# Kernel tuning notes

Hardware: AMD Instinct MI355X
Metric: run time of the kernel (lower is better)

Reference implementation:

```python
import jax, jax.numpy as jnp
import numpy as np

D = 4096
NB = 4
DFF = int(D * (4 / 3))  # 5461
EPS = 1e-5


def _ln(x, g, b):
    mu = jnp.mean(x, axis=-1, keepdims=True)
    var = jnp.var(x, axis=-1, keepdims=True)
    return (x - mu) * jax.lax.rsqrt(var + EPS) * g + b


def setup_inputs() -> dict:
    key = jax.random.key(0)
    ks = jax.random.split(key, 8)
    bs = NB  # blocks
    ib = D // NB
    inp = {
        "x": jax.random.normal(ks[0], (4, 2048, D), jnp.float32),
        "W_gates": jax.random.normal(ks[1], (4, bs, ib, ib), jnp.float32) / np.sqrt(ib),
        "b_gates": jnp.zeros((4, D), jnp.float32),
        "Wr_gates": jax.random.normal(ks[2], (4, bs, ib, ib), jnp.float32) / np.sqrt(ib),
        "ln_gamma": jnp.ones((8, D), jnp.float32),
        "ln_beta": jnp.zeros((8, D), jnp.float32),
        "lnout_gamma": jnp.ones((DFF,), jnp.float32),
        "lnout_beta": jnp.zeros((DFF,), jnp.float32),
        "W_left": jax.random.normal(ks[3], (DFF, D), jnp.float32) / np.sqrt(D),
        "b_left": jnp.zeros((DFF,), jnp.float32),
        "W_right": jax.random.normal(ks[4], (DFF, D), jnp.float32) / np.sqrt(D),
        "b_right": jnp.zeros((DFF,), jnp.float32),
        "W_proj": jax.random.normal(ks[5], (D, DFF), jnp.float32) / np.sqrt(DFF),
        "b_proj": jnp.zeros((D,), jnp.float32),
    }
    return inp


def reference(x, W_gates, b_gates, Wr_gates, ln_gamma, ln_beta,
              lnout_gamma, lnout_beta, W_left, b_left, W_right, b_right,
              W_proj, b_proj):
    B, N, Dm = x.shape
    nb = W_gates.shape[1]
    ib = Dm // nb

    # fresh states (init_states): all zeros
    ht_1 = jnp.zeros((B, N, Dm), x.dtype)

    xa = jax.nn.silu(x)
    xr = xa.reshape(B, N, nb, ib)
    hr = ht_1.reshape(B, N, nb, ib)
    # block-diagonal gate projections for all 4 gates (i, f, o, z) at once
    pre = jnp.einsum('bnki,gkoi->gbnko', xr, W_gates).reshape(4, B, N, Dm)
    pre = pre + jnp.einsum('bnki,gkoi->gbnko', hr, Wr_gates).reshape(4, B, N, Dm)
    pre = pre + b_gates[:, None, None, :]

    log_i = _ln(pre[0], ln_gamma[0], ln_beta[0])  # log of i before stabilization
    log_f = _ln(pre[1], ln_gamma[1], ln_beta[1])
    # stabilizer (mt_1 = 0): m = max(log f + mt_1, log i)
    m = jnp.maximum(log_f, log_i)
    i = jnp.exp(log_i - m)
    f = jnp.exp(log_f - m)

    o = jax.nn.sigmoid(_ln(pre[2], ln_gamma[2], ln_beta[2]))
    z = jnp.tanh(_ln(pre[3], ln_gamma[3], ln_beta[3]))

    # ct_1 = 0, nt_1 = 0
    ct = i * z
    ct = jnp.mean(_ln(ct, ln_gamma[4], ln_beta[4]), axis=(0, 1), keepdims=True)  # [1,1,D]
    nt = i
    nt = jnp.mean(_ln(nt, ln_gamma[5], ln_beta[5]), axis=(0, 1), keepdims=True)  # [1,1,D]

    ht = o * (ct / nt)  # broadcast [B,N,D]
    ht = jnp.mean(_ln(ht, ln_gamma[6], ln_beta[6]), axis=(0, 1), keepdims=True)  # [1,1,D]

    slstm_out = _ln(ht, ln_gamma[7], ln_beta[7])  # GN
    left = slstm_out @ W_left.T + b_left
    right = jax.nn.gelu(slstm_out @ W_right.T + b_right, approximate=False)
    out = _ln(left * right, lnout_gamma, lnout_beta)
    out = out @ W_proj.T + b_proj  # [1,1,hidden]
    return out
```

## Files before the change

kernel.cpp:

```cpp
#include <hip/hip_runtime.h>
#include <hip/hip_bf16.h>
#include <math.h>

#define DMODEL 4096
#define NROWS  8192
#define DFF    5461
#define CHUNK  512
#define NCHUNK 16
#define LNEPS  1e-5f

#define GBM 128
#define GBN 128
#define GBK 32
#define LOSCALE 2048.0f
#define LOINV   4.8828125e-4f

typedef _Float16 h8 __attribute__((ext_vector_type(8)));
typedef _Float16 h4 __attribute__((ext_vector_type(4)));
typedef float floatx4 __attribute__((ext_vector_type(4)));

__device__ inline unsigned short f2bf(float f) {
    unsigned int x = __builtin_bit_cast(unsigned int, f);
    unsigned int r = x + 0x7FFFu + ((x >> 16) & 1u);
    return (unsigned short)(r >> 16);
}
__device__ inline float bf2f(unsigned short u) {
    return __builtin_bit_cast(float, ((unsigned int)u) << 16);
}

#define GLL(gp, lp) __builtin_amdgcn_global_load_lds( \
    (const __attribute__((address_space(1))) void*)(gp), \
    (__attribute__((address_space(3))) void*)(lp), 16, 0, 0)

__global__ __launch_bounds__(256) void silu_split_k(const float* __restrict__ x,
                                                    _Float16* __restrict__ xh,
                                                    _Float16* __restrict__ xl) {
    size_t i = (size_t)blockIdx.x * 256 + threadIdx.x;
    float4 v = ((const float4*)x)[i];
    float s[4];
    s[0] = v.x / (1.f + expf(-v.x));
    s[1] = v.y / (1.f + expf(-v.y));
    s[2] = v.z / (1.f + expf(-v.z));
    s[3] = v.w / (1.f + expf(-v.w));
    h4 hi, lo;
#pragma unroll
    for (int j = 0; j < 4; ++j) {
        _Float16 h = (_Float16)s[j];
        hi[j] = h;
        lo[j] = (_Float16)((s[j] - (float)h) * LOSCALE);
    }
    ((h4*)xh)[i] = hi;
    ((h4*)xl)[i] = lo;
}

__global__ __launch_bounds__(256) void wsplit_k(const float* __restrict__ Wg,
                                                _Float16* __restrict__ wh,
                                                _Float16* __restrict__ wl) {
    size_t i = (size_t)blockIdx.x * 256 + threadIdx.x;
    float4 v = ((const float4*)Wg)[i];
    float s[4] = {v.x, v.y, v.z, v.w};
    h4 hi, lo;
#pragma unroll
    for (int j = 0; j < 4; ++j) {
        _Float16 h = (_Float16)s[j];
        hi[j] = h;
        lo[j] = (_Float16)((s[j] - (float)h) * LOSCALE);
    }
    ((h4*)wh)[i] = hi;
    ((h4*)wl)[i] = lo;
}

__global__ __launch_bounds__(256, 2) void gemm_split_k(
    const _Float16* __restrict__ xh, const _Float16* __restrict__ xl,
    const _Float16* __restrict__ wh, const _Float16* __restrict__ wl,
    float* __restrict__ pre, int row0)
{
    __shared__ __align__(16) _Float16 Ah[GBM * GBK];
    __shared__ __align__(16) _Float16 Al[GBM * GBK];
    __shared__ __align__(16) _Float16 Bh[GBN * GBK];
    __shared__ __align__(16) _Float16 Bl[GBN * GBK];

    const int gz = blockIdx.z;
    const int kb = gz & 3, g = gz >> 2;
    const int tM = blockIdx.y, tN = blockIdx.x;
    const int t = threadIdx.x;
    const int w = t >> 6, l = t & 63;
    const int lane15 = l & 15, quad = l >> 4;
    const int wm = w >> 1, wn = w & 1;

    const size_t Aoff = (size_t)(row0 + tM * GBM) * DMODEL + kb * 1024;
    const size_t Boff = (size_t)gz * (1024 * 1024) + (size_t)(tN * GBN) * 1024;

    floatx4 acc_h[4][4] = {};
    floatx4 acc_x[4][4] = {};

    for (int kt = 0; kt < 1024; kt += GBK) {
        const _Float16* ahs = xh + Aoff + kt;
        const _Float16* als = xl + Aoff + kt;
        const _Float16* bhs = wh + Boff + kt;
        const _Float16* bls = wl + Boff + kt;
#pragma unroll
        for (int it = 0; it < 2; ++it) {
            const int chunk = it * 256 + t;
            const int r = chunk >> 2;
            const int c = (chunk & 3) * 8;
            const int lo = (it * 256 + w * 64) * 8;
            const size_t ga = (size_t)r * DMODEL + c;
            const size_t gb = (size_t)r * 1024 + c;
            GLL(ahs + ga, Ah + lo);
            GLL(als + ga, Al + lo);
            GLL(bhs + gb, Bh + lo);
            GLL(bls + gb, Bl + lo);
        }
        __syncthreads();

        h8 af[4], alf[4], bf[4], blf[4];
#pragma unroll
        for (int mi = 0; mi < 4; ++mi) {
            const int ro = (wm * 64 + mi * 16 + lane15) * GBK + quad * 8;
            af[mi]  = *(const h8*)&Ah[ro];
            alf[mi] = *(const h8*)&Al[ro];
        }
#pragma unroll
        for (int ni = 0; ni < 4; ++ni) {
            const int ro = (wn * 64 + ni * 16 + lane15) * GBK + quad * 8;
            bf[ni]  = *(const h8*)&Bh[ro];
            blf[ni] = *(const h8*)&Bl[ro];
        }
#pragma unroll
        for (int mi = 0; mi < 4; ++mi)
#pragma unroll
            for (int ni = 0; ni < 4; ++ni) {
                acc_h[mi][ni] = __builtin_amdgcn_mfma_f32_16x16x32_f16(
                    af[mi], bf[ni], acc_h[mi][ni], 0, 0, 0);
                acc_x[mi][ni] = __builtin_amdgcn_mfma_f32_16x16x32_f16(
                    af[mi], blf[ni], acc_x[mi][ni], 0, 0, 0);
                acc_x[mi][ni] = __builtin_amdgcn_mfma_f32_16x16x32_f16(
                    alf[mi], bf[ni], acc_x[mi][ni], 0, 0, 0);
            }
        __syncthreads();
    }

#pragma unroll
    for (int mi = 0; mi < 4; ++mi) {
#pragma unroll
        for (int r = 0; r < 4; ++r) {
            const int rowl = tM * GBM + wm * 64 + mi * 16 + quad * 4 + r;
            float* dst = pre + ((size_t)g * CHUNK + rowl) * DMODEL
                         + kb * 1024 + tN * GBN + wn * 64 + lane15;
#pragma unroll
            for (int ni = 0; ni < 4; ++ni)
                dst[ni * 16] = acc_h[mi][ni][r] + acc_x[mi][ni][r] * LOINV;
        }
    }
}

template <int N>
__device__ inline void block_reduce(float* s, float* red) {
    const int t = threadIdx.x, w = t >> 6, l = t & 63;
#pragma unroll
    for (int i = 0; i < N; ++i) {
        float v = s[i];
#pragma unroll
        for (int off = 32; off > 0; off >>= 1) v += __shfl_xor(v, off, 64);
        if (l == 0) red[w * N + i] = v;
    }
    __syncthreads();
#pragma unroll
    for (int i = 0; i < N; ++i)
        s[i] = red[0 * N + i] + red[1 * N + i] + red[2 * N + i] + red[3 * N + i];
    __syncthreads();
}

#define EROWS 2
__global__ __launch_bounds__(256) void lnpass_k(
    const float* __restrict__ pre, const float* __restrict__ bg,
    const float* __restrict__ lng, const float* __restrict__ lnb,
    unsigned short* __restrict__ obuf,
    float* __restrict__ ctv, float* __restrict__ ntv, int row0)
{
    __shared__ float red[32];
    const int t = threadIdx.x;
    const float n1 = 1.f / DMODEL;
    float ct_acc[16] = {}, nt_acc[16] = {};

    for (int rr = 0; rr < EROWS; ++rr) {
        const int rl = blockIdx.x * EROWS + rr;
        const float* p0 = pre + ((size_t)0 * CHUNK + rl) * DMODEL;
        const float* p1 = pre + ((size_t)1 * CHUNK + rl) * DMODEL;
        const float* p2 = pre + ((size_t)2 * CHUNK + rl) * DMODEL;
        const float* p3 = pre + ((size_t)3 * CHUNK + rl) * DMODEL;

        float s[8] = {};
        for (int j = 0; j < 16; ++j) {
            const int d = t + 256 * j;
            float v0 = p0[d] + bg[d];
            float v1 = p1[d] + bg[DMODEL + d];
            float v2 = p2[d] + bg[2 * DMODEL + d];
            float v3 = p3[d] + bg[3 * DMODEL + d];
            s[0] += v0; s[1] += v0 * v0;
            s[2] += v1; s[3] += v1 * v1;
            s[4] += v2; s[5] += v2 * v2;
            s[6] += v3; s[7] += v3 * v3;
        }
        block_reduce<8>(s, red);
        const float mu0 = s[0] * n1, rs0 = rsqrtf(s[1] * n1 - mu0 * mu0 + LNEPS);
        const float mu1 = s[2] * n1, rs1 = rsqrtf(s[3] * n1 - mu1 * mu1 + LNEPS);
        const float mu2 = s[4] * n1, rs2 = rsqrtf(s[5] * n1 - mu2 * mu2 + LNEPS);
        const float mu3 = s[6] * n1, rs3 = rsqrtf(s[7] * n1 - mu3 * mu3 + LNEPS);

        float ctl[16], ntl[16];
        float s2[4] = {};
        for (int j = 0; j < 16; ++j) {
            const int d = t + 256 * j;
            float li = (p0[d] + bg[d] - mu0) * rs0 * lng[d] + lnb[d];
            float lf = (p1[d] + bg[DMODEL + d] - mu1) * rs1 * lng[DMODEL + d] + lnb[DMODEL + d];
            float iv = expf(fminf(li - lf, 0.f));
            float zv = tanhf((p3[d] + bg[3 * DMODEL + d] - mu3) * rs3 * lng[3 * DMODEL + d]
                             + lnb[3 * DMODEL + d]);
            float c = iv * zv;
            ctl[j] = c; ntl[j] = iv;
            s2[0] += c;  s2[1] += c * c;
            s2[2] += iv; s2[3] += iv * iv;
        }
        block_reduce<4>(s2, red);
        const float cmu = s2[0] * n1, crs = rsqrtf(s2[1] * n1 - cmu * cmu + LNEPS);
        const float nmu = s2[2] * n1, nrs = rsqrtf(s2[3] * n1 - nmu * nmu + LNEPS);

        for (int j = 0; j < 16; ++j) {
            const int d = t + 256 * j;
            ct_acc[j] += (ctl[j] - cmu) * crs * lng[4 * DMODEL + d] + lnb[4 * DMODEL + d];
            nt_acc[j] += (ntl[j] - nmu) * nrs * lng[5 * DMODEL + d] + lnb[5 * DMODEL + d];
            float ov = (p2[d] + bg[2 * DMODEL + d] - mu2) * rs2 * lng[2 * DMODEL + d]
                       + lnb[2 * DMODEL + d];
            ov = 1.f / (1.f + expf(-ov));
            obuf[(size_t)(row0 + rl) * DMODEL + d] = f2bf(ov);
        }
    }
    for (int j = 0; j < 16; ++j) {
        const int d = t + 256 * j;
        atomicAdd(&ctv[d], ct_acc[j]);
        atomicAdd(&ntv[d], nt_acc[j]);
    }
}

#define HROWS 16
__global__ __launch_bounds__(256) void htpass_k(
    const unsigned short* __restrict__ obuf,
    const float* __restrict__ ctv, const float* __restrict__ ntv,
    const float* __restrict__ lng, const float* __restrict__ lnb,
    float* __restrict__ htv)
{
    __shared__ float red[8];
    const int t = threadIdx.x;
    const float n1 = 1.f / DMODEL;
    float r[16], hacc[16] = {};
    for (int j = 0; j < 16; ++j) {
        const int d = t + 256 * j;
        r[j] = ctv[d] / ntv[d];
    }
    for (int rr = 0; rr < HROWS; ++rr) {
        const int row = blockIdx.x * HROWS + rr;
        float h[16]; float s[2] = {};
        for (int j = 0; j < 16; ++j) {
            const int d = t + 256 * j;
            h[j] = bf2f(obuf[(size_t)row * DMODEL + d]) * r[j];
            s[0] += h[j]; s[1] += h[j] * h[j];
        }
        block_reduce<2>(s, red);
        const float mu = s[0] * n1, rsv = rsqrtf(s[1] * n1 - mu * mu + LNEPS);
        for (int j = 0; j < 16; ++j) {
            const int d = t + 256 * j;
            hacc[j] += (h[j] - mu) * rsv * lng[6 * DMODEL + d] + lnb[6 * DMODEL + d];
        }
    }
    for (int j = 0; j < 16; ++j) {
        const int d = t + 256 * j;
        atomicAdd(&htv[d], hacc[j]);
    }
}

__global__ __launch_bounds__(256) void finalvec_k(
    const float* __restrict__ htv, const float* __restrict__ lng,
    const float* __restrict__ lnb, float* __restrict__ sout)
{
    __shared__ float red[8];
    const int t = threadIdx.x;
    const float n1 = 1.f / DMODEL;
    float v[16]; float s[2] = {};
    for (int j = 0; j < 16; ++j) {
        const int d = t + 256 * j;
        v[j] = htv[d] * (1.f / (float)NROWS);
        s[0] += v[j]; s[1] += v[j] * v[j];
    }
    block_reduce<2>(s, red);
    const float mu = s[0] * n1, rs = rsqrtf(s[1] * n1 - mu * mu + LNEPS);
    for (int j = 0; j < 16; ++j) {
        const int d = t + 256 * j;
        sout[d] = (v[j] - mu) * rs * lng[7 * DMODEL + d] + lnb[7 * DMODEL + d];
    }
}

__global__ __launch_bounds__(256) void ffn1_k(
    const float* __restrict__ sout,
    const float* __restrict__ Wl, const float* __restrict__ bl,
    const float* __restrict__ Wr, const float* __restrict__ br,
    float* __restrict__ u)
{
    const int t = threadIdx.x, w = t >> 6, l = t & 63;
    const int f = blockIdx.x * 4 + w;
    if (f >= DFF) return;
    const float4* wl4 = (const float4*)(Wl + (size_t)f * DMODEL);
    const float4* wr4 = (const float4*)(Wr + (size_t)f * DMODEL);
    const float4* s4 = (const float4*)sout;
    float a = 0.f, b = 0.f;
#pragma unroll
    for (int jj = 0; jj < 16; ++jj) {
        const int i4 = l + 64 * jj;
        float4 sv = s4[i4], av = wl4[i4], bv = wr4[i4];
        a += sv.x * av.x + sv.y * av.y + sv.z * av.z + sv.w * av.w;
        b += sv.x * bv.x + sv.y * bv.y + sv.z * bv.z + sv.w * bv.w;
    }
#pragma unroll
    for (int off = 32; off > 0; off >>= 1) {
        a += __shfl_xor(a, off, 64);
        b += __shfl_xor(b, off, 64);
    }
    if (l == 0) {
        float lv = a + bl[f];
        float rv = b + br[f];
        float g = 0.5f * rv * (1.f + erff(rv * 0.70710678118654752f));
        u[f] = lv * g;
    }
}

__global__ __launch_bounds__(256) void lnout_k(
    const float* __restrict__ u, const float* __restrict__ g,
    const float* __restrict__ b, float* __restrict__ y)
{
    __shared__ float red[8];
    const int t = threadIdx.x;
    float s[2] = {};
    for (int d = t; d < DFF; d += 256) { float v = u[d]; s[0] += v; s[1] += v * v; }
    block_reduce<2>(s, red);
    const float n1 = 1.f / (float)DFF;
    const float mu = s[0] * n1, rs = rsqrtf(s[1] * n1 - mu * mu + LNEPS);
    for (int d = t; d < DFF; d += 256) y[d] = (u[d] - mu) * rs * g[d] + b[d];
}

__global__ __launch_bounds__(256) void ffn2_k(
    const float* __restrict__ y, const float* __restrict__ Wp,
    const float* __restrict__ bp, float* __restrict__ out)
{
    const int t = threadIdx.x, w = t >> 6, l = t & 63;
    const int d = blockIdx.x * 4 + w;
    const float* row = Wp + (size_t)d * DFF;
    float s = 0.f;
    for (int j = l; j < DFF; j += 64) s += row[j] * y[j];
#pragma unroll
    for (int off = 32; off > 0; off >>= 1) s += __shfl_xor(s, off, 64);
    if (l == 0) out[d] = s + bp[d];
}

extern "C" void kernel_launch(void* const* d_in, const int* in_sizes, int n_in,
                              void* d_out, int out_size, void* d_ws, size_t ws_size,
                              hipStream_t stream)
{
    const float* x   = (const float*)d_in[0];
    const float* Wg  = (const float*)d_in[1];
    const float* bg  = (const float*)d_in[2];
    const float* lng = (const float*)d_in[4];
    const float* lnb = (const float*)d_in[5];
    const float* log_ = (const float*)d_in[6];
    const float* lob  = (const float*)d_in[7];
    const float* Wl  = (const float*)d_in[8];
    const float* bl  = (const float*)d_in[9];
    const float* Wr  = (const float*)d_in[10];
    const float* br  = (const float*)d_in[11];
    const float* Wp  = (const float*)d_in[12];
    const float* bp  = (const float*)d_in[13];
    float* out = (float*)d_out;

    char* ws = (char*)d_ws;
    size_t off = 0;
    _Float16* xh = (_Float16*)(ws + off); off += (size_t)NROWS * DMODEL * 2;
    _Float16* xl = (_Float16*)(ws + off); off += (size_t)NROWS * DMODEL * 2;
    _Float16* whp = (_Float16*)(ws + off); off += (size_t)16 * 1024 * 1024 * 2;
    _Float16* wlp = (_Float16*)(ws + off); off += (size_t)16 * 1024 * 1024 * 2;
    float* pre  = (float*)(ws + off); off += (size_t)4 * CHUNK * DMODEL * 4;
    float* ctv  = (float*)(ws + off); off += DMODEL * 4;
    float* ntv  = (float*)(ws + off); off += DMODEL * 4;
    float* htv  = (float*)(ws + off); off += DMODEL * 4;
    float* sout = (float*)(ws + off); off += DMODEL * 4;
    float* u    = (float*)(ws + off); off += DFF * 4;
    float* y    = (float*)(ws + off); off += DFF * 4;

    unsigned short* obuf = (unsigned short*)xl;

    hipMemsetAsync(ctv, 0, 3 * DMODEL * 4, stream);

    silu_split_k<<<(NROWS * DMODEL) / 1024, 256, 0, stream>>>(x, xh, xl);
    wsplit_k<<<(16 * 1024 * 1024) / 1024, 256, 0, stream>>>(Wg, whp, wlp);

    for (int c = 0; c < NCHUNK; ++c) {
        const int row0 = c * CHUNK;
        dim3 grid(1024 / GBN, CHUNK / GBM, 16);
        gemm_split_k<<<grid, 256, 0, stream>>>(xh, xl, whp, wlp, pre, row0);
        lnpass_k<<<CHUNK / EROWS, 256, 0, stream>>>(pre, bg, lng, lnb, obuf, ctv, ntv, row0);
    }

    htpass_k<<<NROWS / HROWS, 256, 0, stream>>>(obuf, ctv, ntv, lng, lnb, htv);
    finalvec_k<<<1, 256, 0, stream>>>(htv, lng, lnb, sout);
    ffn1_k<<<(DFF + 3) / 4, 256, 0, stream>>>(sout, Wl, bl, Wr, br, u);
    lnout_k<<<1, 256, 0, stream>>>(u, log_, lob, y);
    ffn2_k<<<DMODEL / 4, 256, 0, stream>>>(y, Wp, bp, out);

    (void)in_sizes; (void)n_in; (void)out_size; (void)ws_size;
}
```

Before: 2.636 ms.

## Use 1024-thread row blocks with float4 loads and shadow atomic accumulators

The LN pass and the ht pass now use 1024-thread blocks that handle one row, or four rows for the ht pass, with float4/ushort4 vectorized loads and stores instead of strided scalar accesses. The column accumulators for ct, nt and ht are replicated into four shadow copies indexed by block, so concurrent atomics spread across more addresses; consumers sum the copies. The aim is to cut memory transaction count and atomic contention. In exchange, lnpass issues more atomics in total (one row per block instead of two), and block reductions now span 16 waves.

```diff
diff --git a/kernel.cpp b/kernel.cpp
--- a/kernel.cpp
+++ b/kernel.cpp
@@ -8,6 +8,7 @@
 #define CHUNK  512
 #define NCHUNK 16
 #define LNEPS  1e-5f
+#define NSHADOW 4
 
 #define GBM 128
 #define GBN 128
@@ -156,6 +157,27 @@
 }
 
 template <int N>
+__device__ inline void block_reduce16(float* s, float* red) {
+    const int t = threadIdx.x, w = t >> 6, l = t & 63;
+#pragma unroll
+    for (int i = 0; i < N; ++i) {
+        float v = s[i];
+#pragma unroll
+        for (int off = 32; off > 0; off >>= 1) v += __shfl_xor(v, off, 64);
+        if (l == 0) red[w * N + i] = v;
+    }
+    __syncthreads();
+#pragma unroll
+    for (int i = 0; i < N; ++i) {
+        float acc = 0.f;
+#pragma unroll
+        for (int ww = 0; ww < 16; ++ww) acc += red[ww * N + i];
+        s[i] = acc;
+    }
+    __syncthreads();
+}
+
+template <int N>
 __device__ inline void block_reduce(float* s, float* red) {
     const int t = threadIdx.x, w = t >> 6, l = t & 63;
 #pragma unroll
@@ -172,112 +194,140 @@
     __syncthreads();
 }
 
-#define EROWS 2
-__global__ __launch_bounds__(256) void lnpass_k(
+__global__ __launch_bounds__(1024) void lnpass_k(
     const float* __restrict__ pre, const float* __restrict__ bg,
     const float* __restrict__ lng, const float* __restrict__ lnb,
     unsigned short* __restrict__ obuf,
     float* __restrict__ ctv, float* __restrict__ ntv, int row0)
 {
-    __shared__ float red[32];
+    __shared__ float red[16 * 8];
     const int t = threadIdx.x;
+    const int rl = blockIdx.x;
     const float n1 = 1.f / DMODEL;
-    float ct_acc[16] = {}, nt_acc[16] = {};
-
-    for (int rr = 0; rr < EROWS; ++rr) {
-        const int rl = blockIdx.x * EROWS + rr;
-        const float* p0 = pre + ((size_t)0 * CHUNK + rl) * DMODEL;
-        const float* p1 = pre + ((size_t)1 * CHUNK + rl) * DMODEL;
-        const float* p2 = pre + ((size_t)2 * CHUNK + rl) * DMODEL;
-        const float* p3 = pre + ((size_t)3 * CHUNK + rl) * DMODEL;
-
-        float s[8] = {};
-        for (int j = 0; j < 16; ++j) {
-            const int d = t + 256 * j;
-            float v0 = p0[d] + bg[d];
-            float v1 = p1[d] + bg[DMODEL + d];
-            float v2 = p2[d] + bg[2 * DMODEL + d];
-            float v3 = p3[d] + bg[3 * DMODEL + d];
-            s[0] += v0; s[1] += v0 * v0;
-            s[2] += v1; s[3] += v1 * v1;
-            s[4] += v2; s[5] += v2 * v2;
-            s[6] += v3; s[7] += v3 * v3;
-        }
-        block_reduce<8>(s, red);
-        const float mu0 = s[0] * n1, rs0 = rsqrtf(s[1] * n1 - mu0 * mu0 + LNEPS);
-        const float mu1 = s[2] * n1, rs1 = rsqrtf(s[3] * n1 - mu1 * mu1 + LNEPS);
-        const float mu2 = s[4] * n1, rs2 = rsqrtf(s[5] * n1 - mu2 * mu2 + LNEPS);
-        const float mu3 = s[6] * n1, rs3 = rsqrtf(s[7] * n1 - mu3 * mu3 + LNEPS);
-
-        float ctl[16], ntl[16];
-        float s2[4] = {};
-        for (int j = 0; j < 16; ++j) {
-            const int d = t + 256 * j;
-            float li = (p0[d] + bg[d] - mu0) * rs0 * lng[d] + lnb[d];
-            float lf = (p1[d] + bg[DMODEL + d] - mu1) * rs1 * lng[DMODEL + d] + lnb[DMODEL + d];
-            float iv = expf(fminf(li - lf, 0.f));
-            float zv = tanhf((p3[d] + bg[3 * DMODEL + d] - mu3) * rs3 * lng[3 * DMODEL + d]
-                             + lnb[3 * DMODEL + d]);
-            float c = iv * zv;
-            ctl[j] = c; ntl[j] = iv;
-            s2[0] += c;  s2[1] += c * c;
-            s2[2] += iv; s2[3] += iv * iv;
-        }
-        block_reduce<4>(s2, red);
-        const float cmu = s2[0] * n1, crs = rsqrtf(s2[1] * n1 - cmu * cmu + LNEPS);
-        const float nmu = s2[2] * n1, nrs = rsqrtf(s2[3] * n1 - nmu * nmu + LNEPS);
-
-        for (int j = 0; j < 16; ++j) {
-            const int d = t + 256 * j;
-            ct_acc[j] += (ctl[j] - cmu) * crs * lng[4 * DMODEL + d] + lnb[4 * DMODEL + d];
-            nt_acc[j] += (ntl[j] - nmu) * nrs * lng[5 * DMODEL + d] + lnb[5 * DMODEL + d];
-            float ov = (p2[d] + bg[2 * DMODEL + d] - mu2) * rs2 * lng[2 * DMODEL + d]
-                       + lnb[2 * DMODEL + d];
-            ov = 1.f / (1.f + expf(-ov));
-            obuf[(size_t)(row0 + rl) * DMODEL + d] = f2bf(ov);
-        }
-    }
-    for (int j = 0; j < 16; ++j) {
-        const int d = t + 256 * j;
-        atomicAdd(&ctv[d], ct_acc[j]);
-        atomicAdd(&ntv[d], nt_acc[j]);
-    }
-}
-
-#define HROWS 16
-__global__ __launch_bounds__(256) void htpass_k(
+
+    float v[4][4];
+#pragma unroll
+    for (int g = 0; g < 4; ++g) {
+        float4 pv = ((const float4*)(pre + ((size_t)g * CHUNK + rl) * DMODEL))[t];
+        float4 bv = ((const float4*)bg)[g * (DMODEL / 4) + t];
+        v[g][0] = pv.x + bv.x; v[g][1] = pv.y + bv.y;
+        v[g][2] = pv.z + bv.z; v[g][3] = pv.w + bv.w;
+    }
+
+    float s[8];
+#pragma unroll
+    for (int g = 0; g < 4; ++g) {
+        s[2 * g]     = v[g][0] + v[g][1] + v[g][2] + v[g][3];
+        s[2 * g + 1] = v[g][0] * v[g][0] + v[g][1] * v[g][1]
+                     + v[g][2] * v[g][2] + v[g][3] * v[g][3];
+    }
+    block_reduce16<8>(s, red);
+    const float mu0 = s[0] * n1, rs0 = rsqrtf(s[1] * n1 - mu0 * mu0 + LNEPS);
+    const float mu1 = s[2] * n1, rs1 = rsqrtf(s[3] * n1 - mu1 * mu1 + LNEPS);
+    const float mu2 = s[4] * n1, rs2 = rsqrtf(s[5] * n1 - mu2 * mu2 + LNEPS);
+    const float mu3 = s[6] * n1, rs3 = rsqrtf(s[7] * n1 - mu3 * mu3 + LNEPS);
+
+    float4 g0 = ((const float4*)lng)[0 * (DMODEL / 4) + t], b0 = ((const float4*)lnb)[0 * (DMODEL / 4) + t];
+    float4 g1 = ((const float4*)lng)[1 * (DMODEL / 4) + t], b1 = ((const float4*)lnb)[1 * (DMODEL / 4) + t];
+    float4 g3 = ((const float4*)lng)[3 * (DMODEL / 4) + t], b3 = ((const float4*)lnb)[3 * (DMODEL / 4) + t];
+    const float* g0p = (const float*)&g0; const float* b0p = (const float*)&b0;
+    const float* g1p = (const float*)&g1; const float* b1p = (const float*)&b1;
+    const float* g3p = (const float*)&g3; const float* b3p = (const float*)&b3;
+
+    float cv[4], iv[4];
+    float s2[4] = {};
+#pragma unroll
+    for (int e = 0; e < 4; ++e) {
+        float li = (v[0][e] - mu0) * rs0 * g0p[e] + b0p[e];
+        float lf = (v[1][e] - mu1) * rs1 * g1p[e] + b1p[e];
+        float ii = expf(fminf(li - lf, 0.f));
+        float zz = tanhf((v[3][e] - mu3) * rs3 * g3p[e] + b3p[e]);
+        float cc = ii * zz;
+        cv[e] = cc; iv[e] = ii;
+        s2[0] += cc; s2[1] += cc * cc;
+        s2[2] += ii; s2[3] += ii * ii;
+    }
+    block_reduce16<4>(s2, red);
+    const float cmu = s2[0] * n1, crs = rsqrtf(s2[1] * n1 - cmu * cmu + LNEPS);
+    const float nmu = s2[2] * n1, nrs = rsqrtf(s2[3] * n1 - nmu * nmu + LNEPS);
+
+    float4 g4 = ((const float4*)lng)[4 * (DMODEL / 4) + t], b4 = ((const float4*)lnb)[4 * (DMODEL / 4) + t];
+    float4 g5 = ((const float4*)lng)[5 * (DMODEL / 4) + t], b5 = ((const float4*)lnb)[5 * (DMODEL / 4) + t];
+    float4 g2 = ((const float4*)lng)[2 * (DMODEL / 4) + t], b2 = ((const float4*)lnb)[2 * (DMODEL / 4) + t];
+    const float* g4p = (const float*)&g4; const float* b4p = (const float*)&b4;
+    const float* g5p = (const float*)&g5; const float* b5p = (const float*)&b5;
+    const float* g2p = (const float*)&g2; const float* b2p = (const float*)&b2;
+
+    float cta[4], nta[4];
+    unsigned short ob[4];
+#pragma unroll
+    for (int e = 0; e < 4; ++e) {
+        cta[e] = (cv[e] - cmu) * crs * g4p[e] + b4p[e];
+        nta[e] = (iv[e] - nmu) * nrs * g5p[e] + b5p[e];
+        float ov = (v[2][e] - mu2) * rs2 * g2p[e] + b2p[e];
+        ov = 1.f / (1.f + expf(-ov));
+        ob[e] = f2bf(ov);
+    }
+    ushort4 obv = make_ushort4(ob[0], ob[1], ob[2], ob[3]);
+    ((ushort4*)(obuf + (size_t)(row0 + rl) * DMODEL))[t] = obv;
+
+    const int sh = (blockIdx.x & (NSHADOW - 1)) * DMODEL + 4 * t;
+#pragma unroll
+    for (int e = 0; e < 4; ++e) {
+        atomicAdd(&ctv[sh + e], cta[e]);
+        atomicAdd(&ntv[sh + e], nta[e]);
+    }
+}
+
+#define HROWS 4
+__global__ __launch_bounds__(1024) void htpass_k(
     const unsigned short* __restrict__ obuf,
     const float* __restrict__ ctv, const float* __restrict__ ntv,
     const float* __restrict__ lng, const float* __restrict__ lnb,
     float* __restrict__ htv)
 {
-    __shared__ float red[8];
+    __shared__ float red[16 * 2];
     const int t = threadIdx.x;
     const float n1 = 1.f / DMODEL;
-    float r[16], hacc[16] = {};
-    for (int j = 0; j < 16; ++j) {
-        const int d = t + 256 * j;
-        r[j] = ctv[d] / ntv[d];
-    }
+
+    float r[4];
+    {
+        float4 c0 = ((const float4*)ctv)[0 * (DMODEL / 4) + t];
+        float4 c1 = ((const float4*)ctv)[1 * (DMODEL / 4) + t];
+        float4 c2 = ((const float4*)ctv)[2 * (DMODEL / 4) + t];
+        float4 c3 = ((const float4*)ctv)[3 * (DMODEL / 4) + t];
+        float4 d0 = ((const float4*)ntv)[0 * (DMODEL / 4) + t];
+        float4 d1 = ((const float4*)ntv)[1 * (DMODEL / 4) + t];
+        float4 d2 = ((const float4*)ntv)[2 * (DMODEL / 4) + t];
+        float4 d3 = ((const float4*)ntv)[3 * (DMODEL / 4) + t];
+        r[0] = (c0.x + c1.x + c2.x + c3.x) / (d0.x + d1.x + d2.x + d3.x);
+        r[1] = (c0.y + c1.y + c2.y + c3.y) / (d0.y + d1.y + d2.y + d3.y);
+        r[2] = (c0.z + c1.z + c2.z + c3.z) / (d0.z + d1.z + d2.z + d3.z);
+        r[3] = (c0.w + c1.w + c2.w + c3.w) / (d0.w + d1.w + d2.w + d3.w);
+    }
+    float4 g6 = ((const float4*)lng)[6 * (DMODEL / 4) + t];
+    float4 b6 = ((const float4*)lnb)[6 * (DMODEL / 4) + t];
+    const float* g6p = (const float*)&g6; const float* b6p = (const float*)&b6;
+
+    float hacc[4] = {};
     for (int rr = 0; rr < HROWS; ++rr) {
         const int row = blockIdx.x * HROWS + rr;
-        float h[16]; float s[2] = {};
-        for (int j = 0; j < 16; ++j) {
-            const int d = t + 256 * j;
-            h[j] = bf2f(obuf[(size_t)row * DMODEL + d]) * r[j];
-            s[0] += h[j]; s[1] += h[j] * h[j];
-        }
-        block_reduce<2>(s, red);
+        ushort4 ov = ((const ushort4*)(obuf + (size_t)row * DMODEL))[t];
+        float h[4];
+        h[0] = bf2f(ov.x) * r[0]; h[1] = bf2f(ov.y) * r[1];
+        h[2] = bf2f(ov.z) * r[2]; h[3] = bf2f(ov.w) * r[3];
+        float s[2];
+        s[0] = h[0] + h[1] + h[2] + h[3];
+        s[1] = h[0] * h[0] + h[1] * h[1] + h[2] * h[2] + h[3] * h[3];
+        block_reduce16<2>(s, red);
         const float mu = s[0] * n1, rsv = rsqrtf(s[1] * n1 - mu * mu + LNEPS);
-        for (int j = 0; j < 16; ++j) {
-            const int d = t + 256 * j;
-            hacc[j] += (h[j] - mu) * rsv * lng[6 * DMODEL + d] + lnb[6 * DMODEL + d];
-        }
-    }
-    for (int j = 0; j < 16; ++j) {
-        const int d = t + 256 * j;
-        atomicAdd(&htv[d], hacc[j]);
-    }
+#pragma unroll
+        for (int e = 0; e < 4; ++e)
+            hacc[e] += (h[e] - mu) * rsv * g6p[e] + b6p[e];
+    }
+    const int sh = (blockIdx.x & (NSHADOW - 1)) * DMODEL + 4 * t;
+#pragma unroll
+    for (int e = 0; e < 4; ++e) atomicAdd(&htv[sh + e], hacc[e]);
 }
 
 __global__ __launch_bounds__(256) void finalvec_k(
@@ -290,7 +340,8 @@
     float v[16]; float s[2] = {};
     for (int j = 0; j < 16; ++j) {
         const int d = t + 256 * j;
-        v[j] = htv[d] * (1.f / (float)NROWS);
+        float hv = htv[d] + htv[DMODEL + d] + htv[2 * DMODEL + d] + htv[3 * DMODEL + d];
+        v[j] = hv * (1.f / (float)NROWS);
         s[0] += v[j]; s[1] += v[j] * v[j];
     }
     block_reduce<2>(s, red);
@@ -388,16 +439,16 @@
     _Float16* whp = (_Float16*)(ws + off); off += (size_t)16 * 1024 * 1024 * 2;
     _Float16* wlp = (_Float16*)(ws + off); off += (size_t)16 * 1024 * 1024 * 2;
     float* pre  = (float*)(ws + off); off += (size_t)4 * CHUNK * DMODEL * 4;
-    float* ctv  = (float*)(ws + off); off += DMODEL * 4;
-    float* ntv  = (float*)(ws + off); off += DMODEL * 4;
-    float* htv  = (float*)(ws + off); off += DMODEL * 4;
+    float* ctv  = (float*)(ws + off); off += NSHADOW * DMODEL * 4;
+    float* ntv  = (float*)(ws + off); off += NSHADOW * DMODEL * 4;
+    float* htv  = (float*)(ws + off); off += NSHADOW * DMODEL * 4;
     float* sout = (float*)(ws + off); off += DMODEL * 4;
     float* u    = (float*)(ws + off); off += DFF * 4;
     float* y    = (float*)(ws + off); off += DFF * 4;
 
     unsigned short* obuf = (unsigned short*)xl;
 
-    hipMemsetAsync(ctv, 0, 3 * DMODEL * 4, stream);
+    hipMemsetAsync(ctv, 0, 3 * NSHADOW * DMODEL * 4, stream);
 
     silu_split_k<<<(NROWS * DMODEL) / 1024, 256, 0, stream>>>(x, xh, xl);
     wsplit_k<<<(16 * 1024 * 1024) / 1024, 256, 0, stream>>>(Wg, whp, wlp);
@@ -406,10 +457,10 @@
         const int row0 = c * CHUNK;
         dim3 grid(1024 / GBN, CHUNK / GBM, 16);
         gemm_split_k<<<grid, 256, 0, stream>>>(xh, xl, whp, wlp, pre, row0);
-        lnpass_k<<<CHUNK / EROWS, 256, 0, stream>>>(pre, bg, lng, lnb, obuf, ctv, ntv, row0);
-    }
-
-    htpass_k<<<NROWS / HROWS, 256, 0, stream>>>(obuf, ctv, ntv, lng, lnb, htv);
+        lnpass_k<<<CHUNK, 1024, 0, stream>>>(pre, bg, lng, lnb, obuf, ctv, ntv, row0);
+    }
+
+    htpass_k<<<NROWS / HROWS, 1024, 0, stream>>>(obuf, ctv, ntv, lng, lnb, htv);
     finalvec_k<<<1, 256, 0, stream>>>(htv, lng, lnb, sout);
     ffn1_k<<<(DFF + 3) / 4, 256, 0, stream>>>(sout, Wl, bl, Wr, br, u);
     lnout_k<<<1, 256, 0, stream>>>(u, log_, lob, y);
```

New measurement: 3.403 ms. 29.1% more time.
